# Kernel tuning notes

Hardware: AMD Instinct MI355X
Metric: run time of the kernel (lower is better)

## Reference

```python
import jax, jax.numpy as jnp
import numpy as np

BN_EPS = 1e-5

def _square_distance(src, dst):
    # src [B,N,3], dst [B,S,3] -> [B,N,S]
    d = -2.0 * jnp.einsum('bnc,bsc->bns', src, dst)
    d = d + jnp.sum(src * src, -1)[:, :, None]
    d = d + jnp.sum(dst * dst, -1)[:, None, :]
    return d

def _conv_bn_relu(x, w, b, g, beta):
    # x [B,C,N]; 1x1 conv == channel GEMM, then training-mode batchnorm over (B,N)
    y = jnp.einsum('oc,bcn->bon', w, x) + b[None, :, None]
    mean = jnp.mean(y, axis=(0, 2), keepdims=True)
    var = jnp.mean((y - mean) ** 2, axis=(0, 2), keepdims=True)  # biased, as torch BN uses for normalization
    y = (y - mean) * jax.lax.rsqrt(var + BN_EPS)
    y = y * g[None, :, None] + beta[None, :, None]
    return jax.nn.relu(y)

def setup_inputs() -> dict:
    key = jax.random.key(0)
    ks = jax.random.split(key, 8)
    B, N, S, D1, D2 = 8, 8192, 2048, 128, 256
    C_in, C_mid, C_out = D1 + D2, 256, 256
    return {
        'xyz1': jax.random.normal(ks[0], (B, 3, N), jnp.float32),
        'xyz2': jax.random.normal(ks[1], (B, 3, S), jnp.float32),
        'points1': jax.random.normal(ks[2], (B, D1, N), jnp.float32),
        'points2': jax.random.normal(ks[3], (B, D2, S), jnp.float32),
        'w1': jax.random.normal(ks[4], (C_mid, C_in), jnp.float32) * (1.0 / np.sqrt(C_in)),
        'b1': jax.random.normal(ks[5], (C_mid,), jnp.float32) * 0.01,
        'g1': jnp.ones((C_mid,), jnp.float32),
        'beta1': jnp.zeros((C_mid,), jnp.float32),
        'w2': jax.random.normal(ks[6], (C_out, C_mid), jnp.float32) * (1.0 / np.sqrt(C_mid)),
        'b2': jax.random.normal(ks[7], (C_out,), jnp.float32) * 0.01,
        'g2': jnp.ones((C_out,), jnp.float32),
        'beta2': jnp.zeros((C_out,), jnp.float32),
    }

def reference(xyz1, xyz2, points1, points2, w1, b1, g1, beta1, w2, b2, g2, beta2):
    B = xyz1.shape[0]
    p1xyz = jnp.transpose(xyz1, (0, 2, 1))      # [B,N,3]
    p2xyz = jnp.transpose(xyz2, (0, 2, 1))      # [B,S,3]
    p2 = jnp.transpose(points2, (0, 2, 1))      # [B,S,D2]

    dists = _square_distance(p1xyz, p2xyz)      # [B,N,S]
    neg_d3, idx = jax.lax.top_k(-dists, 3)      # 3 smallest distances
    d3 = -neg_d3                                # [B,N,3]
    recip = 1.0 / (d3 + 1e-8)
    weight = recip / jnp.sum(recip, axis=2, keepdims=True)  # [B,N,3]

    gathered = jax.vmap(lambda p, i: p[i])(p2, idx)          # [B,N,3,D2]
    interp = jnp.sum(gathered * weight[..., None], axis=2)   # [B,N,D2]

    new_points = jnp.concatenate([jnp.transpose(points1, (0, 2, 1)), interp], axis=-1)
    x = jnp.transpose(new_points, (0, 2, 1))    # [B,D1+D2,N]
    x = _conv_bn_relu(x, w1, b1, g1, beta1)
    x = _conv_bn_relu(x, w2, b2, g2, beta2)
    return x
```

## Files before the change

kernel.cpp:

```cpp
#include <hip/hip_runtime.h>

#define B_    8
#define N_    8192
#define S_    2048
#define D1_   128
#define D2_   256
#define CIN_  384
#define CMID_ 256
#define COUT_ 256

typedef unsigned int  u32;
typedef unsigned short u16;
typedef __attribute__((ext_vector_type(8))) short short8;
typedef __attribute__((ext_vector_type(4))) float f32x4;

static __device__ __forceinline__ u32 uminu(u32 a, u32 b) { return a < b ? a : b; }
static __device__ __forceinline__ u32 umed3(u32 a, u32 b, u32 c) {
  u32 d;
  asm("v_med3_u32 %0, %1, %2, %3" : "=v"(d) : "v"(a), "v"(b), "v"(c));
  return d;
}
static __device__ __forceinline__ u16 f2bf(float f) {
  union { float f; u32 u; } v; v.f = f;
  u32 r = v.u + 0x7FFFu + ((v.u >> 16) & 1u);
  return (u16)(r >> 16);
}
static __device__ __forceinline__ float bflo(u32 u) { return __uint_as_float(u << 16); }
static __device__ __forceinline__ float bfhi(u32 u) { return __uint_as_float(u & 0xFFFF0000u); }
static __device__ __forceinline__ u32 cvtpk_bf16(float lo, float hi) {
  u32 d;
  asm("v_cvt_pk_bf16_f32 %0, %1, %2" : "=v"(d) : "v"(lo), "v"(hi));
  return d;
}

#define GLD16(g, l)                                                             \
  __builtin_amdgcn_global_load_lds((const __attribute__((address_space(1))) void*)(g), \
                                   (__attribute__((address_space(3))) void*)(l), 16, 0, 0)

#define WB(N)                                                                   \
  __builtin_amdgcn_sched_barrier(0);                                            \
  asm volatile("s_waitcnt vmcnt(" #N ")" ::: "memory");                         \
  __builtin_amdgcn_s_barrier();                                                 \
  __builtin_amdgcn_sched_barrier(0);

__global__ __launch_bounds__(256) void k_pre(const float* __restrict__ xyz2,
                                             float4* __restrict__ pts4,
                                             const float* __restrict__ w1,
                                             const float* __restrict__ w2,
                                             u16* __restrict__ w1b,
                                             u16* __restrict__ w2b) {
  const int i = blockIdx.x * 256 + threadIdx.x;
  if (i < B_ * S_) {
    const int b = i >> 11, s = i & (S_ - 1);
    const float* xb = xyz2 + (size_t)b * 3 * S_;
    float x = xb[s], y = xb[S_ + s], z = xb[2 * S_ + s];
    pts4[b * S_ + s] = make_float4(-2.f * x, -2.f * y, -2.f * z, x * x + y * y + z * z);
    return;
  }
  const int j = i - B_ * S_;
  if (j < CMID_ * CIN_) { w1b[j] = f2bf(w1[j]); return; }
  const int h = j - CMID_ * CIN_;
  if (h < COUT_ * CMID_) w2b[h] = f2bf(w2[h]);
}

__global__ __launch_bounds__(256) void k_nn_scan(const float* __restrict__ xyz1,
                                                 const float4* __restrict__ pts4,
                                                 uint4* __restrict__ keys) {
  const int b = blockIdx.z, chunk = blockIdx.y;
  const int n = blockIdx.x * 256 + threadIdx.x;
  const float* pb = xyz1 + (size_t)b * 3 * N_;
  const float px = pb[n], py = pb[N_ + n], pz = pb[2 * N_ + n];
  const float pn = px * px + py * py + pz * pz;
  const float4* __restrict__ P = pts4 + b * S_ + chunk * 256;
  u32 m0 = ~0u, m1 = ~0u, m2 = ~0u;
#pragma unroll 8
  for (int s = 0; s < 256; ++s) {
    float4 q = P[s];
    float d = fmaf(px, q.x, fmaf(py, q.y, fmaf(pz, q.z, pn + q.w)));
    d = fmaxf(d, 0.f);
    u32 k = (__float_as_uint(d) & 0xFFFFFF00u) | (u32)s;
    u32 m2n = umed3(m1, m2, k);
    m1 = umed3(m0, m1, k);
    m0 = uminu(m0, k);
    m2 = m2n;
  }
  uint4 v; v.x = m0; v.y = m1; v.z = m2; v.w = m2;
  keys[((size_t)(b * 8 + chunk)) * N_ + n] = v;
}

__global__ __launch_bounds__(256) void k_refine(const float* __restrict__ xyz1,
                                                const float4* __restrict__ pts4,
                                                const uint4* __restrict__ keys,
                                                int4* __restrict__ idx4,
                                                float4* __restrict__ w4) {
  const int b = blockIdx.y, n = blockIdx.x * 256 + threadIdx.x;
  const float* pb = xyz1 + (size_t)b * 3 * N_;
  const double px = (double)pb[n], py = (double)pb[N_ + n], pz = (double)pb[2 * N_ + n];
  const double pn = px * px + py * py + pz * pz;
  double bd0 = 1e300, bd1 = 1e300, bd2 = 1e300;
  int bi0 = 1 << 30, bi1 = 1 << 30, bi2 = 1 << 30;
#pragma unroll
  for (int c = 0; c < 8; ++c) {
    uint4 kk = keys[((size_t)(b * 8 + c)) * N_ + n];
    u32 arr[3] = {kk.x, kk.y, kk.z};
#pragma unroll
    for (int j = 0; j < 3; ++j) {
      int s = c * 256 + (int)(arr[j] & 255u);
      float4 q = pts4[b * S_ + s];
      double x = (double)(q.x * -0.5f), y = (double)(q.y * -0.5f), z = (double)(q.z * -0.5f);
      double dot = px * x + py * y + pz * z;
      double d = -2.0 * dot + (pn + (x * x + y * y + z * z));
      if (d < bd2 || (d == bd2 && s < bi2)) {
        if (d < bd1 || (d == bd1 && s < bi1)) {
          bd2 = bd1; bi2 = bi1;
          if (d < bd0 || (d == bd0 && s < bi0)) { bd1 = bd0; bi1 = bi0; bd0 = d; bi0 = s; }
          else                                  { bd1 = d;  bi1 = s; }
        } else { bd2 = d; bi2 = s; }
      }
    }
  }
  float f0 = (float)bd0, f1 = (float)bd1, f2 = (float)bd2;
  float r0 = 1.f / (f0 + 1e-8f), r1 = 1.f / (f1 + 1e-8f), r2 = 1.f / (f2 + 1e-8f);
  float rs = r0 + r1 + r2;
  w4[(size_t)b * N_ + n]   = make_float4(r0 / rs, r1 / rs, r2 / rs, 0.f);
  idx4[(size_t)b * N_ + n] = make_int4(bi0, bi1, bi2, 0);
}

__global__ __launch_bounds__(256) void k_p2t(const float* __restrict__ p2,
                                             float* __restrict__ p2T) {
  __shared__ float t[32][33];
  const int b = blockIdx.z, s0 = blockIdx.x * 32, d0 = blockIdx.y * 32;
  const int cc = threadIdx.x & 31, rr = threadIdx.x >> 5;
#pragma unroll
  for (int i = 0; i < 4; ++i) {
    int r = rr + i * 8;
    t[r][cc] = p2[((size_t)b * D2_ + d0 + r) * S_ + s0 + cc];
  }
  __syncthreads();
#pragma unroll
  for (int i = 0; i < 4; ++i) {
    int r = rr + i * 8;
    p2T[((size_t)b * S_ + s0 + r) * D2_ + d0 + cc] = t[cc][r];
  }
}

__global__ __launch_bounds__(256) void k_packp1(const float* __restrict__ p1,
                                                u16* __restrict__ xT) {
  __shared__ float t[32][33];
  const int b = blockIdx.z, n0 = blockIdx.x * 32, c0 = blockIdx.y * 32;
  const int cc = threadIdx.x & 31, rr = threadIdx.x >> 5;
#pragma unroll
  for (int i = 0; i < 4; ++i) {
    int r = rr + i * 8;
    t[r][cc] = p1[((size_t)b * D1_ + c0 + r) * N_ + n0 + cc];
  }
  __syncthreads();
#pragma unroll
  for (int i = 0; i < 4; ++i) {
    int r = rr + i * 8;
    xT[((size_t)b * N_ + n0 + r) * CIN_ + c0 + cc] = f2bf(t[cc][r]);
  }
}

__global__ __launch_bounds__(256) void k_gather_pack(const float* __restrict__ p2T,
                                                     const int4* __restrict__ idx4,
                                                     const float4* __restrict__ w4,
                                                     u16* __restrict__ xT) {
  const int b = blockIdx.y;
  const int wv = threadIdx.x >> 6, lane = threadIdx.x & 63;
  const int nbase = blockIdx.x * 16 + wv * 4;
  int4   id[4];
  float4 w[4];
#pragma unroll
  for (int i = 0; i < 4; ++i) {
    id[i] = idx4[(size_t)b * N_ + nbase + i];
    w[i]  = w4[(size_t)b * N_ + nbase + i];
  }
#pragma unroll
  for (int i = 0; i < 4; ++i) {
    const int n = nbase + i;
    const float4* r0 = (const float4*)(p2T + ((size_t)b * S_ + id[i].x) * D2_) + lane;
    const float4* r1 = (const float4*)(p2T + ((size_t)b * S_ + id[i].y) * D2_) + lane;
    const float4* r2 = (const float4*)(p2T + ((size_t)b * S_ + id[i].z) * D2_) + lane;
    float4 a = *r0, bb = *r1, cq = *r2;
    ushort4 pk;
    pk.x = f2bf(a.x * w[i].x + bb.x * w[i].y + cq.x * w[i].z);
    pk.y = f2bf(a.y * w[i].x + bb.y * w[i].y + cq.y * w[i].z);
    pk.z = f2bf(a.z * w[i].x + bb.z * w[i].y + cq.z * w[i].z);
    pk.w = f2bf(a.w * w[i].x + bb.w * w[i].y + cq.w * w[i].z);
    *(ushort4*)(xT + ((size_t)b * N_ + n) * CIN_ + D1_ + lane * 4) = pk;
  }
}

__global__ __launch_bounds__(64) void k_bnstat(const float* __restrict__ ps,
                                               const float* __restrict__ pq,
                                               const float* __restrict__ g,
                                               const float* __restrict__ beta,
                                               float* __restrict__ scale,
                                               float* __restrict__ shift) {
  const int o = blockIdx.x, l = threadIdx.x;
  float s = 0.f, q = 0.f;
#pragma unroll
  for (int i = 0; i < 8; ++i) {
    s += ps[(size_t)(i * 64 + l) * 256 + o];
    q += pq[(size_t)(i * 64 + l) * 256 + o];
  }
#pragma unroll
  for (int m = 1; m <= 32; m <<= 1) { s += __shfl_xor(s, m); q += __shfl_xor(q, m); }
  if (l == 0) {
    const float inv = 1.0f / (float)(B_ * N_);
    float mean = s * inv;
    float var = q * inv - mean * mean;
    float sc = g[o] / sqrtf(var + 1e-5f);
    scale[o] = sc;
    shift[o] = beta[o] - mean * sc;
  }
}

__global__ __launch_bounds__(512) void k_gemm1(const u16* __restrict__ Wb,
                                               const float* __restrict__ bias,
                                               const u16* __restrict__ xT,
                                               u16* __restrict__ y1T,
                                               float* __restrict__ psum,
                                               float* __restrict__ pssq) {
  __shared__ u16 As[3][8192];
  __shared__ u16 Bs[3][4096];
  __shared__ float s_sum[256], s_ssq[256];
  const int b = blockIdx.z, bn0 = blockIdx.x * 128;
  const int tid = threadIdx.x, w = tid >> 6, l = tid & 63;
  const int wm = w & 3, wn = w >> 2;
  const int lr = l >> 2, lc = l & 3;
  const int fm = l & 15, fq = l >> 4;
  const int clog = (lc ^ ((lr >> 1) & 3)) * 8;
  const int swz8 = (fq ^ ((fm >> 1) & 3)) * 8;
  f32x4 acc[4][4];
#pragma unroll
  for (int i = 0; i < 4; ++i)
#pragma unroll
    for (int j = 0; j < 4; ++j) acc[i][j] = (f32x4){0.f, 0.f, 0.f, 0.f};

  const int NK = CIN_ / 32;

#define STAGE1(kk, buf)                                                         \
  {                                                                             \
    const int k0_ = (kk) * 32;                                                  \
    _Pragma("unroll") for (int j_ = 0; j_ < 2; ++j_) {                          \
      int seg_ = w * 2 + j_, row_ = seg_ * 16 + lr;                             \
      GLD16(Wb + (size_t)row_ * CIN_ + k0_ + clog, &As[buf][seg_ * 512]);       \
    }                                                                           \
    int brow_ = w * 16 + lr;                                                    \
    GLD16(xT + ((size_t)b * N_ + bn0 + brow_) * CIN_ + k0_ + clog,              \
          &Bs[buf][w * 512]);                                                   \
  }

  STAGE1(0, 0);
  STAGE1(1, 1);
  int cur = 0;
  for (int kk = 0; kk < NK; ++kk) {
    if (kk + 1 < NK) { WB(3) } else { WB(0) }
    if (kk + 2 < NK) {
      int bt = cur + 2; if (bt >= 3) bt -= 3;
      STAGE1(kk + 2, bt);
    }
    short8 af[4], bfr[4];
#pragma unroll
    for (int f = 0; f < 4; ++f) {
      af[f]  = *(const short8*)&As[cur][(wm * 64 + f * 16 + fm) * 32 + swz8];
      bfr[f] = *(const short8*)&Bs[cur][(wn * 64 + f * 16 + fm) * 32 + swz8];
    }
#pragma unroll
    for (int i = 0; i < 4; ++i)
#pragma unroll
      for (int j = 0; j < 4; ++j)
        acc[i][j] = __builtin_amdgcn_mfma_f32_16x16x32_bf16(af[i], bfr[j], acc[i][j], 0, 0, 0);
    ++cur; if (cur == 3) cur = 0;
  }
#undef STAGE1

  if (tid < 256) { s_sum[tid] = 0.f; s_ssq[tid] = 0.f; }
  __syncthreads();
  u16* tb = y1T + ((size_t)b * 64 + (bn0 >> 7)) * 32768;
#pragma unroll
  for (int i = 0; i < 4; ++i) {
    int ob = wm * 64 + i * 16 + fq * 4;
    float4 b4 = *(const float4*)(bias + ob);
    float sv0 = 0, sv1 = 0, sv2 = 0, sv3 = 0, qv0 = 0, qv1 = 0, qv2 = 0, qv3 = 0;
#pragma unroll
    for (int j = 0; j < 4; ++j) {
      int nl = wn * 64 + j * 16 + fm;
      ushort4 pk;
      pk.x = f2bf(acc[i][j][0] + b4.x);
      pk.y = f2bf(acc[i][j][1] + b4.y);
      pk.z = f2bf(acc[i][j][2] + b4.z);
      pk.w = f2bf(acc[i][j][3] + b4.w);
      *(ushort4*)(tb + (size_t)(ob >> 5) * 4096 + nl * 32 + (ob & 31)) = pk;
      float v0 = bflo(pk.x), v1 = bflo(pk.y), v2 = bflo(pk.z), v3 = bflo(pk.w);
      sv0 += v0; sv1 += v1; sv2 += v2; sv3 += v3;
      qv0 = fmaf(v0, v0, qv0); qv1 = fmaf(v1, v1, qv1);
      qv2 = fmaf(v2, v2, qv2); qv3 = fmaf(v3, v3, qv3);
    }
#pragma unroll
    for (int m = 1; m <= 8; m <<= 1) {
      sv0 += __shfl_xor(sv0, m); sv1 += __shfl_xor(sv1, m);
      sv2 += __shfl_xor(sv2, m); sv3 += __shfl_xor(sv3, m);
      qv0 += __shfl_xor(qv0, m); qv1 += __shfl_xor(qv1, m);
      qv2 += __shfl_xor(qv2, m); qv3 += __shfl_xor(qv3, m);
    }
    if (fm == 0) {
      atomicAdd(&s_sum[ob + 0], sv0); atomicAdd(&s_sum[ob + 1], sv1);
      atomicAdd(&s_sum[ob + 2], sv2); atomicAdd(&s_sum[ob + 3], sv3);
      atomicAdd(&s_ssq[ob + 0], qv0); atomicAdd(&s_ssq[ob + 1], qv1);
      atomicAdd(&s_ssq[ob + 2], qv2); atomicAdd(&s_ssq[ob + 3], qv3);
    }
  }
  __syncthreads();
  if (tid < 256) {
    const int blk = blockIdx.x + 64 * blockIdx.z;
    psum[(size_t)blk * 256 + tid] = s_sum[tid];
    pssq[(size_t)blk * 256 + tid] = s_ssq[tid];
  }
}

__global__ __launch_bounds__(512) void k_gemm2(const u16* __restrict__ Wb2,
                                               const float* __restrict__ b2,
                                               const u16* __restrict__ y1T,
                                               const float* __restrict__ scale,
                                               const float* __restrict__ shift,
                                               u16* __restrict__ y2T,
                                               float* __restrict__ psum,
                                               float* __restrict__ pssq) {
  __shared__ u16 As[3][8192];
  __shared__ u16 Bs[3][4096];
  __shared__ float s_sum[256], s_ssq[256];
  __shared__ float s_sc[CMID_], s_sh[CMID_];
  const int b = blockIdx.z, bn0 = blockIdx.x * 128;
  const int tid = threadIdx.x, w = tid >> 6, l = tid & 63;
  const int wm = w & 3, wn = w >> 2;
  const int lr = l >> 2, lc = l & 3;
  const int fm = l & 15, fq = l >> 4;
  const int clog = (lc ^ ((lr >> 1) & 3)) * 8;
  const int swz8 = (fq ^ ((fm >> 1) & 3)) * 8;
  if (tid < 256) {
    s_sc[tid] = scale[tid];
    s_sh[tid] = shift[tid];
  }
  f32x4 acc[4][4];
#pragma unroll
  for (int i = 0; i < 4; ++i)
#pragma unroll
    for (int j = 0; j < 4; ++j) acc[i][j] = (f32x4){0.f, 0.f, 0.f, 0.f};

  const u16* tb = y1T + ((size_t)b * 64 + (bn0 >> 7)) * 32768;
  const int NK = CMID_ / 32;

#define STAGE2(kk, buf)                                                         \
  {                                                                             \
    const int k0_ = (kk) * 32;                                                  \
    _Pragma("unroll") for (int j_ = 0; j_ < 2; ++j_) {                          \
      int seg_ = w * 2 + j_, row_ = seg_ * 16 + lr;                             \
      GLD16(Wb2 + (size_t)row_ * CMID_ + k0_ + clog, &As[buf][seg_ * 512]);     \
    }                                                                           \
    int brow_ = w * 16 + lr;                                                    \
    GLD16(tb + (size_t)(kk) * 4096 + brow_ * 32 + clog, &Bs[buf][w * 512]);     \
  }

  STAGE2(0, 0);
  STAGE2(1, 1);
  int cur = 0;
  for (int kk = 0; kk < NK; ++kk) {
    if (kk + 1 < NK) { WB(3) } else { WB(0) }
    if (kk + 2 < NK) {
      int bt = cur + 2; if (bt >= 3) bt -= 3;
      STAGE2(kk + 2, bt);
    }
    const int kb = kk * 32 + fq * 8;
    float4 s0 = *(const float4*)&s_sc[kb], s1 = *(const float4*)&s_sc[kb + 4];
    float4 h0 = *(const float4*)&s_sh[kb], h1 = *(const float4*)&s_sh[kb + 4];
    short8 af[4], bfr[4];
#pragma unroll
    for (int f = 0; f < 4; ++f) {
      af[f] = *(const short8*)&As[cur][(wm * 64 + f * 16 + fm) * 32 + swz8];
      uint4 r = *(const uint4*)&Bs[cur][(wn * 64 + f * 16 + fm) * 32 + swz8];
      float v0 = fmaxf(fmaf(bflo(r.x), s0.x, h0.x), 0.f);
      float v1 = fmaxf(fmaf(bfhi(r.x), s0.y, h0.y), 0.f);
      float v2 = fmaxf(fmaf(bflo(r.y), s0.z, h0.z), 0.f);
      float v3 = fmaxf(fmaf(bfhi(r.y), s0.w, h0.w), 0.f);
      float v4 = fmaxf(fmaf(bflo(r.z), s1.x, h1.x), 0.f);
      float v5 = fmaxf(fmaf(bfhi(r.z), s1.y, h1.y), 0.f);
      float v6 = fmaxf(fmaf(bflo(r.w), s1.z, h1.z), 0.f);
      float v7 = fmaxf(fmaf(bfhi(r.w), s1.w, h1.w), 0.f);
      union { u32 u[4]; short8 s; } cv;
      cv.u[0] = cvtpk_bf16(v0, v1); cv.u[1] = cvtpk_bf16(v2, v3);
      cv.u[2] = cvtpk_bf16(v4, v5); cv.u[3] = cvtpk_bf16(v6, v7);
      bfr[f] = cv.s;
    }
#pragma unroll
    for (int i = 0; i < 4; ++i)
#pragma unroll
      for (int j = 0; j < 4; ++j)
        acc[i][j] = __builtin_amdgcn_mfma_f32_16x16x32_bf16(af[i], bfr[j], acc[i][j], 0, 0, 0);
    ++cur; if (cur == 3) cur = 0;
  }
#undef STAGE2

  if (tid < 256) { s_sum[tid] = 0.f; s_ssq[tid] = 0.f; }
  __syncthreads();
  u16* tb2 = y2T + ((size_t)b * 64 + (bn0 >> 7)) * 32768;
#pragma unroll
  for (int i = 0; i < 4; ++i) {
    int ob = wm * 64 + i * 16 + fq * 4;
    float4 b4 = *(const float4*)(b2 + ob);
    float sv0 = 0, sv1 = 0, sv2 = 0, sv3 = 0, qv0 = 0, qv1 = 0, qv2 = 0, qv3 = 0;
#pragma unroll
    for (int j = 0; j < 4; ++j) {
      int nl = wn * 64 + j * 16 + fm;
      ushort4 pk;
      pk.x = f2bf(acc[i][j][0] + b4.x);
      pk.y = f2bf(acc[i][j][1] + b4.y);
      pk.z = f2bf(acc[i][j][2] + b4.z);
      pk.w = f2bf(acc[i][j][3] + b4.w);
      *(ushort4*)(tb2 + (size_t)(ob >> 5) * 4096 + nl * 32 + (ob & 31)) = pk;
      float v0 = bflo(pk.x), v1 = bflo(pk.y), v2 = bflo(pk.z), v3 = bflo(pk.w);
      sv0 += v0; sv1 += v1; sv2 += v2; sv3 += v3;
      qv0 = fmaf(v0, v0, qv0); qv1 = fmaf(v1, v1, qv1);
      qv2 = fmaf(v2, v2, qv2); qv3 = fmaf(v3, v3, qv3);
    }
#pragma unroll
    for (int m = 1; m <= 8; m <<= 1) {
      sv0 += __shfl_xor(sv0, m); sv1 += __shfl_xor(sv1, m);
      sv2 += __shfl_xor(sv2, m); sv3 += __shfl_xor(sv3, m);
      qv0 += __shfl_xor(qv0, m); qv1 += __shfl_xor(qv1, m);
      qv2 += __shfl_xor(qv2, m); qv3 += __shfl_xor(qv3, m);
    }
    if (fm == 0) {
      atomicAdd(&s_sum[ob + 0], sv0); atomicAdd(&s_sum[ob + 1], sv1);
      atomicAdd(&s_sum[ob + 2], sv2); atomicAdd(&s_sum[ob + 3], sv3);
      atomicAdd(&s_ssq[ob + 0], qv0); atomicAdd(&s_ssq[ob + 1], qv1);
      atomicAdd(&s_ssq[ob + 2], qv2); atomicAdd(&s_ssq[ob + 3], qv3);
    }
  }
  __syncthreads();
  if (tid < 256) {
    const int blk = blockIdx.x + 64 * blockIdx.z;
    psum[(size_t)blk * 256 + tid] = s_sum[tid];
    pssq[(size_t)blk * 256 + tid] = s_ssq[tid];
  }
}

__global__ __launch_bounds__(256) void k_bn2t(const u16* __restrict__ y2T,
                                              const float* __restrict__ scale,
                                              const float* __restrict__ shift,
                                              float* __restrict__ out) {
  __shared__ float t[32][33];
  const int b = blockIdx.z, n0 = blockIdx.x * 32, o0 = blockIdx.y * 32;
  const int cc = threadIdx.x & 31, rr = threadIdx.x >> 5;
  const float sc = scale[o0 + cc], sh = shift[o0 + cc];
  const u16* tb = y2T + ((size_t)b * 64 + (n0 >> 7)) * 32768 +
                  (size_t)(o0 >> 5) * 4096 + (size_t)(n0 & 96) * 32;
#pragma unroll
  for (int i = 0; i < 4; ++i) {
    int r = rr + i * 8;
    float v = bflo((u32)tb[r * 32 + cc]);
    t[r][cc] = fmaxf(fmaf(v, sc, sh), 0.f);
  }
  __syncthreads();
#pragma unroll
  for (int i = 0; i < 4; ++i) {
    int r = rr + i * 8;
    out[((size_t)b * COUT_ + o0 + r) * N_ + n0 + cc] = t[cc][r];
  }
}

extern "C" void kernel_launch(void* const* d_in, const int* in_sizes, int n_in,
                              void* d_out, int out_size, void* d_ws, size_t ws_size,
                              hipStream_t stream) {
  const float* xyz1    = (const float*)d_in[0];
  const float* xyz2    = (const float*)d_in[1];
  const float* points1 = (const float*)d_in[2];
  const float* points2 = (const float*)d_in[3];
  const float* w1      = (const float*)d_in[4];
  const float* b1      = (const float*)d_in[5];
  const float* g1      = (const float*)d_in[6];
  const float* beta1   = (const float*)d_in[7];
  const float* w2      = (const float*)d_in[8];
  const float* b2      = (const float*)d_in[9];
  const float* g2      = (const float*)d_in[10];
  const float* beta2   = (const float*)d_in[11];
  float* out = (float*)d_out;

  char* ws = (char*)d_ws;
  size_t off = 0;
  u16*    xT    = (u16*)(ws + off);    off += (size_t)B_ * N_ * CIN_ * 2;
  u16*    y1T   = (u16*)(ws + off);    off += (size_t)B_ * N_ * CMID_ * 2;
  float*  p2T   = (float*)(ws + off);  off += (size_t)B_ * S_ * D2_ * 4;
  float4* pts4  = (float4*)(ws + off); off += (size_t)B_ * S_ * 16;
  uint4*  keys  = (uint4*)(ws + off);  off += (size_t)B_ * 8 * N_ * 16;
  int4*   idx4  = (int4*)(ws + off);   off += (size_t)B_ * N_ * 16;
  float4* w4    = (float4*)(ws + off); off += (size_t)B_ * N_ * 16;
  u16*    w1b   = (u16*)(ws + off);    off += (size_t)CMID_ * CIN_ * 2;
  u16*    w2b   = (u16*)(ws + off);    off += (size_t)COUT_ * CMID_ * 2;
  float*  stats = (float*)(ws + off);  off += 1024 * sizeof(float);
  u16*    y2T   = xT;
  float* psum1 = (float*)keys;
  float* pssq1 = psum1 + 256 * 512;
  float* psum2 = pssq1 + 256 * 512;
  float* pssq2 = psum2 + 256 * 512;
  float* scale1 = stats,        * shift1 = stats + 256;
  float* scale2 = stats + 512,  * shift2 = stats + 768;

  k_pre        <<<dim3((B_ * S_ + CMID_ * CIN_ + COUT_ * CMID_) / 256), 256, 0, stream>>>(
                   xyz2, pts4, w1, w2, w1b, w2b);
  k_p2t        <<<dim3(S_ / 32, D2_ / 32, B_), 256, 0, stream>>>(points2, p2T);
  k_nn_scan    <<<dim3(N_ / 256, 8, B_), 256, 0, stream>>>(xyz1, pts4, keys);
  k_refine     <<<dim3(N_ / 256, B_), 256, 0, stream>>>(xyz1, pts4, keys, idx4, w4);
  k_packp1     <<<dim3(N_ / 32, D1_ / 32, B_), 256, 0, stream>>>(points1, xT);
  k_gather_pack<<<dim3(N_ / 16, B_), 256, 0, stream>>>(p2T, idx4, w4, xT);
  k_gemm1      <<<dim3(N_ / 128, 1, B_), 512, 0, stream>>>(w1b, b1, xT, y1T,
                                                           psum1, pssq1);
  k_bnstat     <<<dim3(CMID_), 64, 0, stream>>>(psum1, pssq1, g1, beta1, scale1, shift1);
  k_gemm2      <<<dim3(N_ / 128, 1, B_), 512, 0, stream>>>(w2b, b2, y1T,
                                                           scale1, shift1,
                                                           y2T, psum2, pssq2);
  k_bnstat     <<<dim3(COUT_), 64, 0, stream>>>(psum2, pssq2, g2, beta2, scale2, shift2);
  k_bn2t       <<<dim3(N_ / 32, COUT_ / 32, B_), 256, 0, stream>>>(y2T, scale2, shift2, out);
}
```

Before: 273.4 us.

## Fuse nearest-neighbour scan with refinement and merge preprocessing kernels into one launch

Each thread now scans all source points in four 512-point chunks and runs the double-precision refinement directly, instead of writing per-chunk top-3 keys to global memory for a separate refine kernel. This removes the keys buffer traffic and one launch, but the scan grid shrinks eightfold, so each CU runs far fewer waves with longer serial loops. Packed keys also keep one fewer distance bit, which leaves more ties for the refinement to settle. Separately, the points2 transpose, the points1 pack and the weight/xyz preprocessing are merged into one launch that dispatches on block ranges.

```diff
diff --git a/kernel.cpp b/kernel.cpp
--- a/kernel.cpp
+++ b/kernel.cpp
@@ -43,13 +43,51 @@
   __builtin_amdgcn_s_barrier();                                                 \
   __builtin_amdgcn_sched_barrier(0);
 
-__global__ __launch_bounds__(256) void k_pre(const float* __restrict__ xyz2,
-                                             float4* __restrict__ pts4,
-                                             const float* __restrict__ w1,
-                                             const float* __restrict__ w2,
-                                             u16* __restrict__ w1b,
-                                             u16* __restrict__ w2b) {
-  const int i = blockIdx.x * 256 + threadIdx.x;
+__global__ __launch_bounds__(256) void k_pre_all(const float* __restrict__ xyz2,
+                                                 float4* __restrict__ pts4,
+                                                 const float* __restrict__ w1,
+                                                 const float* __restrict__ w2,
+                                                 u16* __restrict__ w1b,
+                                                 u16* __restrict__ w2b,
+                                                 const float* __restrict__ p2,
+                                                 float* __restrict__ p2T,
+                                                 const float* __restrict__ p1,
+                                                 u16* __restrict__ xT) {
+  __shared__ float t[32][33];
+  const int blk = blockIdx.x;
+  const int cc = threadIdx.x & 31, rr = threadIdx.x >> 5;
+  if (blk < 4096) {
+    const int s0 = (blk & 63) * 32, d0 = ((blk >> 6) & 7) * 32, b = blk >> 9;
+#pragma unroll
+    for (int i = 0; i < 4; ++i) {
+      int r = rr + i * 8;
+      t[r][cc] = p2[((size_t)b * D2_ + d0 + r) * S_ + s0 + cc];
+    }
+    __syncthreads();
+#pragma unroll
+    for (int i = 0; i < 4; ++i) {
+      int r = rr + i * 8;
+      p2T[((size_t)b * S_ + s0 + r) * D2_ + d0 + cc] = t[cc][r];
+    }
+    return;
+  }
+  if (blk < 12288) {
+    const int idx = blk - 4096;
+    const int n0 = (idx & 255) * 32, c0 = ((idx >> 8) & 3) * 32, b = idx >> 10;
+#pragma unroll
+    for (int i = 0; i < 4; ++i) {
+      int r = rr + i * 8;
+      t[r][cc] = p1[((size_t)b * D1_ + c0 + r) * N_ + n0 + cc];
+    }
+    __syncthreads();
+#pragma unroll
+    for (int i = 0; i < 4; ++i) {
+      int r = rr + i * 8;
+      xT[((size_t)b * N_ + n0 + r) * CIN_ + c0 + cc] = f2bf(t[cc][r]);
+    }
+    return;
+  }
+  const int i = (blk - 12288) * 256 + threadIdx.x;
   if (i < B_ * S_) {
     const int b = i >> 11, s = i & (S_ - 1);
     const float* xb = xyz2 + (size_t)b * 3 * S_;
@@ -63,53 +101,41 @@
   if (h < COUT_ * CMID_) w2b[h] = f2bf(w2[h]);
 }
 
-__global__ __launch_bounds__(256) void k_nn_scan(const float* __restrict__ xyz1,
-                                                 const float4* __restrict__ pts4,
-                                                 uint4* __restrict__ keys) {
-  const int b = blockIdx.z, chunk = blockIdx.y;
-  const int n = blockIdx.x * 256 + threadIdx.x;
+__global__ __launch_bounds__(256) void k_nnref(const float* __restrict__ xyz1,
+                                               const float4* __restrict__ pts4,
+                                               int4* __restrict__ idx4,
+                                               float4* __restrict__ w4) {
+  const int b = blockIdx.y, n = blockIdx.x * 256 + threadIdx.x;
   const float* pb = xyz1 + (size_t)b * 3 * N_;
   const float px = pb[n], py = pb[N_ + n], pz = pb[2 * N_ + n];
   const float pn = px * px + py * py + pz * pz;
-  const float4* __restrict__ P = pts4 + b * S_ + chunk * 256;
-  u32 m0 = ~0u, m1 = ~0u, m2 = ~0u;
-#pragma unroll 8
-  for (int s = 0; s < 256; ++s) {
-    float4 q = P[s];
-    float d = fmaf(px, q.x, fmaf(py, q.y, fmaf(pz, q.z, pn + q.w)));
-    d = fmaxf(d, 0.f);
-    u32 k = (__float_as_uint(d) & 0xFFFFFF00u) | (u32)s;
-    u32 m2n = umed3(m1, m2, k);
-    m1 = umed3(m0, m1, k);
-    m0 = uminu(m0, k);
-    m2 = m2n;
-  }
-  uint4 v; v.x = m0; v.y = m1; v.z = m2; v.w = m2;
-  keys[((size_t)(b * 8 + chunk)) * N_ + n] = v;
-}
-
-__global__ __launch_bounds__(256) void k_refine(const float* __restrict__ xyz1,
-                                                const float4* __restrict__ pts4,
-                                                const uint4* __restrict__ keys,
-                                                int4* __restrict__ idx4,
-                                                float4* __restrict__ w4) {
-  const int b = blockIdx.y, n = blockIdx.x * 256 + threadIdx.x;
-  const float* pb = xyz1 + (size_t)b * 3 * N_;
-  const double px = (double)pb[n], py = (double)pb[N_ + n], pz = (double)pb[2 * N_ + n];
-  const double pn = px * px + py * py + pz * pz;
+  const double dpx = (double)px, dpy = (double)py, dpz = (double)pz;
+  const double dpn = dpx * dpx + dpy * dpy + dpz * dpz;
   double bd0 = 1e300, bd1 = 1e300, bd2 = 1e300;
   int bi0 = 1 << 30, bi1 = 1 << 30, bi2 = 1 << 30;
 #pragma unroll
-  for (int c = 0; c < 8; ++c) {
-    uint4 kk = keys[((size_t)(b * 8 + c)) * N_ + n];
-    u32 arr[3] = {kk.x, kk.y, kk.z};
+  for (int chunk = 0; chunk < 4; ++chunk) {
+    const float4* __restrict__ P = pts4 + b * S_ + chunk * 512;
+    u32 m0 = ~0u, m1 = ~0u, m2 = ~0u;
+#pragma unroll 8
+    for (int s = 0; s < 512; ++s) {
+      float4 q = P[s];
+      float d = fmaf(px, q.x, fmaf(py, q.y, fmaf(pz, q.z, pn + q.w)));
+      d = fmaxf(d, 0.f);
+      u32 k = (__float_as_uint(d) & 0xFFFFFE00u) | (u32)s;
+      u32 m2n = umed3(m1, m2, k);
+      m1 = umed3(m0, m1, k);
+      m0 = uminu(m0, k);
+      m2 = m2n;
+    }
+    u32 arr[3] = {m0, m1, m2};
 #pragma unroll
     for (int j = 0; j < 3; ++j) {
-      int s = c * 256 + (int)(arr[j] & 255u);
+      int s = chunk * 512 + (int)(arr[j] & 511u);
       float4 q = pts4[b * S_ + s];
       double x = (double)(q.x * -0.5f), y = (double)(q.y * -0.5f), z = (double)(q.z * -0.5f);
-      double dot = px * x + py * y + pz * z;
-      double d = -2.0 * dot + (pn + (x * x + y * y + z * z));
+      double dot = dpx * x + dpy * y + dpz * z;
+      double d = -2.0 * dot + (dpn + (x * x + y * y + z * z));
       if (d < bd2 || (d == bd2 && s < bi2)) {
         if (d < bd1 || (d == bd1 && s < bi1)) {
           bd2 = bd1; bi2 = bi1;
@@ -124,42 +150,6 @@
   float rs = r0 + r1 + r2;
   w4[(size_t)b * N_ + n]   = make_float4(r0 / rs, r1 / rs, r2 / rs, 0.f);
   idx4[(size_t)b * N_ + n] = make_int4(bi0, bi1, bi2, 0);
-}
-
-__global__ __launch_bounds__(256) void k_p2t(const float* __restrict__ p2,
-                                             float* __restrict__ p2T) {
-  __shared__ float t[32][33];
-  const int b = blockIdx.z, s0 = blockIdx.x * 32, d0 = blockIdx.y * 32;
-  const int cc = threadIdx.x & 31, rr = threadIdx.x >> 5;
-#pragma unroll
-  for (int i = 0; i < 4; ++i) {
-    int r = rr + i * 8;
-    t[r][cc] = p2[((size_t)b * D2_ + d0 + r) * S_ + s0 + cc];
-  }
-  __syncthreads();
-#pragma unroll
-  for (int i = 0; i < 4; ++i) {
-    int r = rr + i * 8;
-    p2T[((size_t)b * S_ + s0 + r) * D2_ + d0 + cc] = t[cc][r];
-  }
-}
-
-__global__ __launch_bounds__(256) void k_packp1(const float* __restrict__ p1,
-                                                u16* __restrict__ xT) {
-  __shared__ float t[32][33];
-  const int b = blockIdx.z, n0 = blockIdx.x * 32, c0 = blockIdx.y * 32;
-  const int cc = threadIdx.x & 31, rr = threadIdx.x >> 5;
-#pragma unroll
-  for (int i = 0; i < 4; ++i) {
-    int r = rr + i * 8;
-    t[r][cc] = p1[((size_t)b * D1_ + c0 + r) * N_ + n0 + cc];
-  }
-  __syncthreads();
-#pragma unroll
-  for (int i = 0; i < 4; ++i) {
-    int r = rr + i * 8;
-    xT[((size_t)b * N_ + n0 + r) * CIN_ + c0 + cc] = f2bf(t[cc][r]);
-  }
 }
 
 __global__ __launch_bounds__(256) void k_gather_pack(const float* __restrict__ p2T,
@@ -494,26 +484,23 @@
   u16*    y1T   = (u16*)(ws + off);    off += (size_t)B_ * N_ * CMID_ * 2;
   float*  p2T   = (float*)(ws + off);  off += (size_t)B_ * S_ * D2_ * 4;
   float4* pts4  = (float4*)(ws + off); off += (size_t)B_ * S_ * 16;
-  uint4*  keys  = (uint4*)(ws + off);  off += (size_t)B_ * 8 * N_ * 16;
   int4*   idx4  = (int4*)(ws + off);   off += (size_t)B_ * N_ * 16;
   float4* w4    = (float4*)(ws + off); off += (size_t)B_ * N_ * 16;
   u16*    w1b   = (u16*)(ws + off);    off += (size_t)CMID_ * CIN_ * 2;
   u16*    w2b   = (u16*)(ws + off);    off += (size_t)COUT_ * CMID_ * 2;
   float*  stats = (float*)(ws + off);  off += 1024 * sizeof(float);
+  float*  psx   = (float*)(ws + off);  off += (size_t)4 * 512 * 256 * 4;
   u16*    y2T   = xT;
-  float* psum1 = (float*)keys;
-  float* pssq1 = psum1 + 256 * 512;
-  float* psum2 = pssq1 + 256 * 512;
-  float* pssq2 = psum2 + 256 * 512;
+  float* psum1 = psx;
+  float* pssq1 = psum1 + 512 * 256;
+  float* psum2 = pssq1 + 512 * 256;
+  float* pssq2 = psum2 + 512 * 256;
   float* scale1 = stats,        * shift1 = stats + 256;
   float* scale2 = stats + 512,  * shift2 = stats + 768;
 
-  k_pre        <<<dim3((B_ * S_ + CMID_ * CIN_ + COUT_ * CMID_) / 256), 256, 0, stream>>>(
-                   xyz2, pts4, w1, w2, w1b, w2b);
-  k_p2t        <<<dim3(S_ / 32, D2_ / 32, B_), 256, 0, stream>>>(points2, p2T);
-  k_nn_scan    <<<dim3(N_ / 256, 8, B_), 256, 0, stream>>>(xyz1, pts4, keys);
-  k_refine     <<<dim3(N_ / 256, B_), 256, 0, stream>>>(xyz1, pts4, keys, idx4, w4);
-  k_packp1     <<<dim3(N_ / 32, D1_ / 32, B_), 256, 0, stream>>>(points1, xT);
+  k_pre_all    <<<dim3(12992), 256, 0, stream>>>(xyz2, pts4, w1, w2, w1b, w2b,
+                                                 points2, p2T, points1, xT);
+  k_nnref      <<<dim3(N_ / 256, B_), 256, 0, stream>>>(xyz1, pts4, idx4, w4);
   k_gather_pack<<<dim3(N_ / 16, B_), 256, 0, stream>>>(p2T, idx4, w4, xT);
   k_gemm1      <<<dim3(N_ / 128, 1, B_), 512, 0, stream>>>(w1b, b1, xT, y1T,
                                                            psum1, pssq1);
```

Result: slower. 326.8 us (+19.5%).
